# Performance work log

Measured on AMD Instinct MI355X. Metric: run time of the kernel, lower is better.

The kernel has to match this reference:

```python
import jax, jax.numpy as jnp
import numpy as np

GROUPS = 32
EPS = 1e-5


def group_norm(x, w, b):
    # x: [B, C, H, W]
    B, C, H, W = x.shape
    g = x.reshape(B, GROUPS, C // GROUPS, H * W)
    mu = g.mean(axis=(2, 3), keepdims=True)
    var = g.var(axis=(2, 3), keepdims=True)
    g = (g - mu) * jax.lax.rsqrt(var + EPS)
    g = g.reshape(B, C, H, W)
    return g * w[None, :, None, None] + b[None, :, None, None]


def setup_inputs() -> dict:
    key = jax.random.key(0)
    ks = jax.random.split(key, 6)
    B, C, H, W = 4, 512, 64, 64
    s = 1.0 / np.sqrt(C)  # sane init scale for 1x1 conv weights
    return {
        "x": jax.random.normal(ks[0], (B, C, H, W), dtype=jnp.float32),
        "gn_w": jnp.ones((C,), dtype=jnp.float32),
        "gn_b": jnp.zeros((C,), dtype=jnp.float32),
        "wq": jax.random.normal(ks[1], (C, C), dtype=jnp.float32) * s,
        "bq": jnp.zeros((C,), dtype=jnp.float32),
        "wk": jax.random.normal(ks[2], (C, C), dtype=jnp.float32) * s,
        "bk": jnp.zeros((C,), dtype=jnp.float32),
        "wv": jax.random.normal(ks[3], (C, C), dtype=jnp.float32) * s,
        "bv": jnp.zeros((C,), dtype=jnp.float32),
        "wp": jax.random.normal(ks[4], (C, C), dtype=jnp.float32) * s,
        "bp": jnp.zeros((C,), dtype=jnp.float32),
    }


def reference(x, gn_w, gn_b, wq, bq, wk, bk, wv, bv, wp, bp):
    B, C, H, W = x.shape
    h = group_norm(x, gn_w, gn_b)
    # tokens: [B, N, C], N = H*W
    t = h.reshape(B, C, H * W).transpose(0, 2, 1)
    # 1x1 convs == per-token linear: y_d = sum_c w[d,c] * t_c + b_d
    q = jnp.einsum('bnc,dc->bnd', t, wq) + bq
    k = jnp.einsum('bnc,dc->bnd', t, wk) + bk
    v = jnp.einsum('bnc,dc->bnd', t, wv) + bv
    scale = 1.0 / jnp.sqrt(jnp.asarray(C, dtype=x.dtype))
    qk = jnp.einsum('bnd,bmd->bnm', q, k) * scale  # [B, N, N]
    attn = jax.nn.softmax(qk, axis=-1)
    out = jnp.einsum('bnm,bmd->bnd', attn, v)  # [B, N, C]
    proj = jnp.einsum('bnc,dc->bnd', out, wp) + bp
    return x + proj.transpose(0, 2, 1).reshape(B, C, H, W)
```

## Files before the change

kernel.cpp:

```cpp
#include <hip/hip_runtime.h>
#include <stdint.h>

#define B_   4
#define C_   512
#define N_   4096
#define G_   32
#define CPG  16
#define EPS  1e-5f

typedef __attribute__((ext_vector_type(8))) short bf16x8;
typedef __attribute__((ext_vector_type(4))) float f32x4;
typedef __attribute__((ext_vector_type(4))) int   i32x4;

__device__ __forceinline__ unsigned short f2bf(float f){
  union { float f; uint32_t u; } v; v.f = f;
  uint32_t r = v.u + 0x7fffu + ((v.u >> 16) & 1u);
  return (unsigned short)(r >> 16);
}
__device__ __forceinline__ float bf2f(unsigned short h){
  union { uint32_t u; float f; } v; v.u = ((uint32_t)h) << 16;
  return v.f;
}

__device__ __forceinline__ void gload16(const unsigned short* g, unsigned short* l){
  __builtin_amdgcn_global_load_lds(
      (__attribute__((address_space(1))) void*)(g),
      (__attribute__((address_space(3))) void*)(l), 16, 0, 0);
}
__device__ __forceinline__ void gload16i(const signed char* g, signed char* l){
  __builtin_amdgcn_global_load_lds(
      (__attribute__((address_space(1))) void*)(g),
      (__attribute__((address_space(3))) void*)(l), 16, 0, 0);
}

__global__ __launch_bounds__(256) void cvt_kernel(const float* __restrict__ in,
                                                  unsigned short* __restrict__ out, int n){
  int i = (blockIdx.x * 256 + threadIdx.x) * 4;
  if (i < n){
    float4 v = *(const float4*)(in + i);
    out[i+0] = f2bf(v.x); out[i+1] = f2bf(v.y);
    out[i+2] = f2bf(v.z); out[i+3] = f2bf(v.w);
  }
}

__global__ __launch_bounds__(256) void cvt_perm_k(const float* __restrict__ in,
                                                  unsigned short* __restrict__ out, int n){
  int i = (blockIdx.x * 256 + threadIdx.x) * 4;
  if (i < n){
    #pragma unroll
    for (int j = 0; j < 4; j++){
      int idx = i + j;
      int row = idx >> 9, col = idx & 511;
      int o = col & 63;
      int sc = (col & ~63) | (((o & 3) << 4) | (o >> 2));
      out[idx] = f2bf(in[(row << 9) | sc]);
    }
  }
}

__global__ __launch_bounds__(256) void concat_bias_k(const float* __restrict__ bq,
                                                     const float* __restrict__ bk,
                                                     const float* __restrict__ bv,
                                                     float* __restrict__ b){
  int i = blockIdx.x * 256 + threadIdx.x;
  if (i < 1536)
    b[i] = (i < 512) ? bq[i] : ((i < 1024) ? bk[i-512] : bv[i-1024]);
}

__global__ __launch_bounds__(256) void gn_stats_k(const float* __restrict__ x,
                                                  float* __restrict__ stats){
  int bg = blockIdx.x;
  const float* p = x + (size_t)bg * (CPG * N_);
  float s = 0.f, ss = 0.f;
  for (int i = threadIdx.x * 4; i < CPG * N_; i += 256 * 4){
    float4 v = *(const float4*)(p + i);
    s  += v.x + v.y + v.z + v.w;
    ss += v.x*v.x + v.y*v.y + v.z*v.z + v.w*v.w;
  }
  #pragma unroll
  for (int o = 32; o >= 1; o >>= 1){ s += __shfl_xor(s, o); ss += __shfl_xor(ss, o); }
  __shared__ float sb[8];
  int w = threadIdx.x >> 6;
  if ((threadIdx.x & 63) == 0){ sb[w] = s; sb[4+w] = ss; }
  __syncthreads();
  if (threadIdx.x == 0){
    float S  = sb[0]+sb[1]+sb[2]+sb[3];
    float SS = sb[4]+sb[5]+sb[6]+sb[7];
    const float inv = 1.f / (CPG * N_);
    float mu  = S * inv;
    float var = SS * inv - mu * mu;
    stats[bg*2]   = mu;
    stats[bg*2+1] = rsqrtf(var + EPS);
  }
}

__global__ __launch_bounds__(256) void gn_apply_k(const float* __restrict__ x,
                                                  const float* __restrict__ stats,
                                                  const float* __restrict__ gw,
                                                  const float* __restrict__ gb,
                                                  unsigned short* __restrict__ t){
  int b  = blockIdx.z;
  int c0 = blockIdx.y * 64, n0 = blockIdx.x * 64;
  __shared__ float tile[64][65];
  for (int i = threadIdx.x; i < 64*64; i += 256){
    int cl = i >> 6, nl = i & 63;
    int c = c0 + cl;
    int g = c >> 4;
    float mu = stats[(b*G_+g)*2], rs = stats[(b*G_+g)*2+1];
    float v = x[((size_t)b*C_ + c)*N_ + n0 + nl];
    tile[cl][nl] = (v - mu) * rs * gw[c] + gb[c];
  }
  __syncthreads();
  for (int i = threadIdx.x; i < 64*64; i += 256){
    int nl = i >> 6, cl = i & 63;
    t[((size_t)b*N_ + n0 + nl)*C_ + c0 + cl] = f2bf(tile[cl][nl]);
  }
}

__global__ __launch_bounds__(256) void transpose_q8_k(const unsigned short* __restrict__ in,
                                                      signed char* __restrict__ out,
                                                      float invs){
  int r0 = blockIdx.x * 64, c0 = blockIdx.y * 64;
  size_t base_in  = (size_t)blockIdx.z * N_ * 1536;
  size_t base_out = (size_t)blockIdx.z * C_ * N_;
  __shared__ signed char tile[64][68];
  for (int i = threadIdx.x; i < 4096; i += 256){
    int rl = i >> 6, cl = i & 63;
    float v = bf2f(in[base_in + (size_t)(r0+rl)*1536 + c0 + cl]);
    int q = __float2int_rn(v * invs);
    tile[rl][cl] = (signed char)max(-127, min(127, q));
  }
  __syncthreads();
  for (int i = threadIdx.x; i < 4096; i += 256){
    int cl = i >> 6, rl = i & 63;
    int rp = ((rl & 15) << 2) | (rl >> 4);
    out[base_out + (size_t)(c0+cl)*N_ + r0 + rp] = tile[rl][cl];
  }
}

__global__ __launch_bounds__(512, 2) void gemm256_k(const unsigned short* __restrict__ A,
                                                    const unsigned short* __restrict__ Bm,
                                                    unsigned short* __restrict__ Cm,
                                                    int lda, int ldb, int ldc,
                                                    int kper, int zdiv, int Mb,
                                                    long long sA, long long sB,
                                                    long long sC, long long sSp,
                                                    const float* __restrict__ bias,
                                                    float scale, int mode,
                                                    signed char* __restrict__ q8p,
                                                    signed char* __restrict__ k8p,
                                                    float invqs){
  __shared__ unsigned short As[2][256*64];
  __shared__ unsigned short Bs[2][256*64];

  const int tid  = threadIdx.x;
  const int lane = tid & 63, wave = tid >> 6;
  const int wr = wave >> 2, wc = wave & 3;
  const int fr = lane & 15, kl = lane >> 4;
  const int kl8 = kl * 8;
  const int rsw = (fr & 7) << 3;

  const int gx = gridDim.x, gy = gridDim.y;
  const int nwg = gx * gy * gridDim.z;
  int bid = blockIdx.x + gx * (blockIdx.y + gy * blockIdx.z);
  if ((nwg & 7) == 0)
    bid = (bid & 7) * (nwg >> 3) + (bid >> 3);
  const int bx = bid % gx;
  const int tmp2 = bid / gx;
  const int by = tmp2 % gy;
  const int bz = tmp2 / gy;

  const int batch = bz / zdiv;
  const int sp    = bz % zdiv;
  const int koff  = sp * kper;
  const unsigned short* Ab = A  + (size_t)batch*sA + (size_t)bx * 256 * lda + koff;
  const unsigned short* Bb = Bm + (size_t)batch*sB + (size_t)by * 256 * ldb + koff;
  unsigned short*       Cb = Cm + (size_t)batch*sC + (size_t)sp*sSp;

  const int g_row = tid >> 3;
  const int g_col = ((tid & 7) * 8) ^ (((tid >> 3) & 7) << 3);
  const int lw    = wave * 512;

#define STAGE(matG, ld, ldsArr, h, kt) do {                                         \
    const unsigned short* _g0 = (matG) + (size_t)((h)*128 + g_row)*(ld)             \
                                + (size_t)(kt)*64 + g_col;                          \
    gload16(_g0,                    &ldsArr[(kt)&1][(h)*8192 + lw]);                \
    gload16(_g0 + (size_t)64*(ld),  &ldsArr[(kt)&1][(h)*8192 + 4096 + lw]);         \
  } while(0)

  f32x4 acc[8][4];
  #pragma unroll
  for (int m = 0; m < 8; m++)
    #pragma unroll
    for (int n = 0; n < 4; n++)
      acc[m][n] = (f32x4){0.f,0.f,0.f,0.f};

  const int NT = kper >> 6;

  STAGE(Ab, lda, As, 0, 0);  STAGE(Ab, lda, As, 1, 0);
  STAGE(Bb, ldb, Bs, 0, 0);  STAGE(Bb, ldb, Bs, 1, 0);
  STAGE(Bb, ldb, Bs, 0, 1);  STAGE(Bb, ldb, Bs, 1, 1);
  asm volatile("s_waitcnt vmcnt(4)" ::: "memory");
  __builtin_amdgcn_sched_barrier(0);
  __builtin_amdgcn_s_barrier();

  bf16x8 af[4][2], ag[4][2], bfr[2][2], bf2[2][2];

#define RD_A(dst, Tl, mhofs)                                                     \
    _Pragma("unroll")                                                            \
    for (int m = 0; m < 4; m++)                                                  \
      _Pragma("unroll")                                                          \
      for (int kk = 0; kk < 2; kk++)                                             \
        dst[m][kk] = *(const bf16x8*)&Tl[(wr*128 + (mhofs) + m*16 + fr)*64 + ((kk*32 + kl8) ^ rsw)];
#define RD_B(dst, Tl, nofs)                                                      \
    _Pragma("unroll")                                                            \
    for (int n = 0; n < 2; n++)                                                  \
      _Pragma("unroll")                                                          \
      for (int kk = 0; kk < 2; kk++)                                             \
        dst[n][kk] = *(const bf16x8*)&Tl[(wc*64 + (nofs) + n*16 + fr)*64 + ((kk*32 + kl8) ^ rsw)];
#define MFMA16(mbase, nbase, afr, bft)                                           \
    __builtin_amdgcn_s_setprio(1);                                               \
    _Pragma("unroll")                                                            \
    for (int m = 0; m < 4; m++)                                                  \
      _Pragma("unroll")                                                          \
      for (int n = 0; n < 2; n++)                                                \
        _Pragma("unroll")                                                        \
        for (int kk = 0; kk < 2; kk++)                                           \
          acc[(mbase)+m][(nbase)+n] = __builtin_amdgcn_mfma_f32_16x16x32_bf16(   \
              afr[m][kk], bft[n][kk], acc[(mbase)+m][(nbase)+n], 0,0,0);         \
    __builtin_amdgcn_s_setprio(0);
#define BAR_LGKM                                                                 \
    __builtin_amdgcn_s_barrier();                                                \
    asm volatile("s_waitcnt lgkmcnt(0)" ::: "memory");                           \
    __builtin_amdgcn_sched_barrier(0);

  for (int kt = 0; kt < NT; kt += 2){
    const unsigned short* __restrict__ Al0 = As[0];
    const unsigned short* __restrict__ Bl0 = Bs[0];
    const unsigned short* __restrict__ Al1 = As[1];
    const unsigned short* __restrict__ Bl1 = Bs[1];

    RD_A(af, Al0, 0)
    RD_B(bfr, Bl0, 0)
    STAGE(Ab, lda, As, 0, kt+1);
    BAR_LGKM
    MFMA16(0, 0, af, bfr)
    __builtin_amdgcn_s_barrier();

    RD_B(bf2, Bl0, 32)
    STAGE(Ab, lda, As, 1, kt+1);
    BAR_LGKM
    MFMA16(0, 2, af, bf2)
    __builtin_amdgcn_s_barrier();

    RD_A(ag, Al0, 64)
    if (kt+2 < NT) STAGE(Bb, ldb, Bs, 0, kt+2);
    BAR_LGKM
    MFMA16(4, 0, ag, bfr)
    __builtin_amdgcn_s_barrier();

    if (kt+2 < NT){
      STAGE(Bb, ldb, Bs, 1, kt+2);
      asm volatile("s_waitcnt vmcnt(4)" ::: "memory");
    } else {
      asm volatile("s_waitcnt vmcnt(0)" ::: "memory");
    }
    __builtin_amdgcn_sched_barrier(0);
    __builtin_amdgcn_s_barrier();
    __builtin_amdgcn_sched_barrier(0);
    MFMA16(4, 2, ag, bf2)
    __builtin_amdgcn_s_barrier();

    RD_A(af, Al1, 0)
    RD_B(bfr, Bl1, 0)
    if (kt+2 < NT) STAGE(Ab, lda, As, 0, kt+2);
    BAR_LGKM
    MFMA16(0, 0, af, bfr)
    __builtin_amdgcn_s_barrier();

    RD_B(bf2, Bl1, 32)
    if (kt+2 < NT) STAGE(Ab, lda, As, 1, kt+2);
    BAR_LGKM
    MFMA16(0, 2, af, bf2)
    __builtin_amdgcn_s_barrier();

    RD_A(ag, Al1, 64)
    if (kt+3 < NT) STAGE(Bb, ldb, Bs, 0, kt+3);
    BAR_LGKM
    MFMA16(4, 0, ag, bfr)
    __builtin_amdgcn_s_barrier();

    if (kt+3 < NT){
      STAGE(Bb, ldb, Bs, 1, kt+3);
      asm volatile("s_waitcnt vmcnt(4)" ::: "memory");
    } else {
      asm volatile("s_waitcnt vmcnt(0)" ::: "memory");
    }
    __builtin_amdgcn_sched_barrier(0);
    __builtin_amdgcn_s_barrier();
    __builtin_amdgcn_sched_barrier(0);
    MFMA16(4, 2, ag, bf2)
    __builtin_amdgcn_s_barrier();
  }
#undef BAR_LGKM
#undef MFMA16
#undef RD_B
#undef RD_A
#undef STAGE

  const int cr = kl * 4, cc = fr;
  if (mode == 3 && by < 4){
    signed char* dst = (by < 2) ? q8p : k8p;
    const int cb = (by & 1)*256 + wc*64 + cc*4;
    #pragma unroll
    for (int m = 0; m < 8; m++){
      #pragma unroll
      for (int r = 0; r < 4; r++){
        int gr = bx*256 + wr*128 + m*16 + cr + r;
        uint32_t pk = 0;
        #pragma unroll
        for (int n = 0; n < 4; n++){
          int gc = by*256 + wc*64 + n*16 + cc;
          float v = (acc[m][n][r] + bias[gc]) * invqs;
          int q = __float2int_rn(v);
          q = max(-127, min(127, q));
          pk |= (uint32_t)(q & 0xff) << (n*8);
        }
        *(uint32_t*)&dst[(size_t)gr*512 + cb] = pk;
      }
    }
  } else {
    #pragma unroll
    for (int m = 0; m < 8; m++){
      #pragma unroll
      for (int n = 0; n < 4; n++){
        int gc = by*256 + wc*64 + n*16 + cc;
        float bv = (mode == 1 || mode == 3) ? bias[gc] : 0.f;
        #pragma unroll
        for (int r = 0; r < 4; r++){
          int gr = bx*256 + wr*128 + m*16 + cr + r;
          Cb[(size_t)gr*ldc + gc] = f2bf((acc[m][n][r] + bv) * scale);
        }
      }
    }
  }
}

__global__ __launch_bounds__(256, 4) void gemm128i_k(const signed char* __restrict__ A,
                                                     const signed char* __restrict__ Bm,
                                                     void* __restrict__ Cv,
                                                     int lda, int ldb, int ldc,
                                                     int kper, int Mb,
                                                     long long sA, long long sB, long long sC,
                                                     float c1, float c2, int mode,
                                                     float* __restrict__ lpart, int lrows,
                                                     const float* __restrict__ linv){
  __shared__ signed char As[128*128];
  __shared__ signed char Bs[128*128];

  const int tid  = threadIdx.x;
  const int lane = tid & 63, wave = tid >> 6;
  const int wr = wave >> 1, wc = wave & 1;
  const int fr = lane & 15, kl = lane >> 4;
  const int rs = fr & 7;

  const int gx = gridDim.x, gy = gridDim.y;
  const int nwg = gx * gy * gridDim.z;
  int bid = blockIdx.x + gx * (blockIdx.y + gy * blockIdx.z);
  if ((nwg & 7) == 0)
    bid = (bid & 7) * (nwg >> 3) + (bid >> 3);
  const int bx = bid % gx;
  const int tmp2 = bid / gx;
  const int by = tmp2 % gy;
  const int batch = tmp2 / gy;

  const signed char* Ab = A  + (size_t)batch*sA + (size_t)bx * 128 * lda;
  const signed char* Bb = Bm + (size_t)batch*sB + (size_t)by * 128 * ldb;

  const int srow = tid >> 3;
  const int gcol = ((tid & 7) ^ ((tid >> 3) & 7)) * 16;
  const signed char* gA = Ab + (size_t)srow * lda + gcol;
  const signed char* gB = Bb + (size_t)srow * ldb + gcol;
  signed char* lA = &As[srow * 128 + (tid & 7) * 16];
  signed char* lB = &Bs[srow * 128 + (tid & 7) * 16];

  i32x4 acc[4][4];
  #pragma unroll
  for (int m = 0; m < 4; m++)
    #pragma unroll
    for (int n = 0; n < 4; n++)
      acc[m][n] = (i32x4){0,0,0,0};

  const int NT = kper >> 7;

  for (int kt = 0; kt < NT; kt++){
    #pragma unroll
    for (int p = 0; p < 4; p++){
      gload16i(gA + (size_t)(p*32)*lda + (size_t)kt*128, lA + p*4096);
      gload16i(gB + (size_t)(p*32)*ldb + (size_t)kt*128, lB + p*4096);
    }
    __syncthreads();
    i32x4 af[4][2], bf[4][2];
    #pragma unroll
    for (int m = 0; m < 4; m++)
      #pragma unroll
      for (int kk = 0; kk < 2; kk++)
        af[m][kk] = *(const i32x4*)&As[(wr*64 + m*16 + fr)*128 + (((kk*4 + kl) ^ rs) << 4)];
    #pragma unroll
    for (int n = 0; n < 4; n++)
      #pragma unroll
      for (int kk = 0; kk < 2; kk++)
        bf[n][kk] = *(const i32x4*)&Bs[(wc*64 + n*16 + fr)*128 + (((kk*4 + kl) ^ rs) << 4)];
    #pragma unroll
    for (int m = 0; m < 4; m++)
      #pragma unroll
      for (int n = 0; n < 4; n++)
        #pragma unroll
        for (int kk = 0; kk < 2; kk++)
          acc[m][n] = __builtin_amdgcn_mfma_i32_16x16x64_i8(af[m][kk], bf[n][kk], acc[m][n], 0,0,0);
    __syncthreads();
  }

  const int cr = kl * 4, cc = fr;
  if (mode == 2){
    signed char* Cb = (signed char*)Cv + (size_t)batch*sC;
    const int cb = by*128 + wc*64 + cc*4;
    const int slice = by*2 + wc;
    #pragma unroll
    for (int m = 0; m < 4; m++){
      #pragma unroll
      for (int r = 0; r < 4; r++){
        int gr = bx*128 + wr*64 + m*16 + cr + r;
        uint32_t pk = 0;
        int ip = 0;
        #pragma unroll
        for (int n = 0; n < 4; n++){
          float arg = (float)acc[m][n][r] * c1 + c2;
          arg = fminf(arg, 6.99f);
          float p = exp2f(arg);
          int pq = (int)(p + 0.5f);
          pk |= (uint32_t)pq << (n*8);
          ip += pq;
        }
        *(uint32_t*)&Cb[(size_t)gr*ldc + cb] = pk;
        float v = (float)ip;
        v += __shfl_xor(v, 1); v += __shfl_xor(v, 2);
        v += __shfl_xor(v, 4); v += __shfl_xor(v, 8);
        if (cc == 0)
          lpart[(size_t)slice * lrows + batch*Mb + gr] = v;
      }
    }
  } else {
    unsigned short* Cb = (unsigned short*)Cv + (size_t)batch*sC;
    const int cb = by*128 + wc*64 + cc*4;
    #pragma unroll
    for (int m = 0; m < 4; m++){
      #pragma unroll
      for (int r = 0; r < 4; r++){
        int gr = bx*128 + wr*64 + m*16 + cr + r;
        float li = linv[batch*Mb + gr] * c1;
        unsigned short w0 = f2bf((float)acc[m][0][r] * li);
        unsigned short w1 = f2bf((float)acc[m][1][r] * li);
        unsigned short w2 = f2bf((float)acc[m][2][r] * li);
        unsigned short w3 = f2bf((float)acc[m][3][r] * li);
        uint2 pk;
        pk.x = (uint32_t)w0 | ((uint32_t)w1 << 16);
        pk.y = (uint32_t)w2 | ((uint32_t)w3 << 16);
        *(uint2*)&Cb[(size_t)gr*ldc + cb] = pk;
      }
    }
  }
}

__global__ __launch_bounds__(256, 2) void gemm_bt_k(const unsigned short* __restrict__ A,
                                                    const unsigned short* __restrict__ Bm,
                                                    unsigned short* __restrict__ Cm,
                                                    int M, int N, int K, int lda, int ldb,
                                                    const float* __restrict__ bias,
                                                    float scale){
  __shared__ unsigned short As[128*32];
  __shared__ unsigned short Bs[128*32];
  const int tid  = threadIdx.x;
  const int lane = tid & 63, wave = tid >> 6;
  const int wr = wave >> 1, wc = wave & 1;

  const int gx = gridDim.x, gy = gridDim.y;
  const int nwg = gx * gy;
  int bid = blockIdx.x + gx * blockIdx.y;
  if ((nwg & 7) == 0)
    bid = (bid & 7) * (nwg >> 3) + (bid >> 3);
  const int bx = bid % gx;
  const int by = bid / gx;

  const unsigned short* Ab = A  + (size_t)bx * 128 * lda;
  const unsigned short* Bb = Bm + (size_t)by * 128 * ldb;

  f32x4 acc[4][4];
  #pragma unroll
  for (int i = 0; i < 4; i++)
    #pragma unroll
    for (int j = 0; j < 4; j++)
      acc[i][j] = (f32x4){0.f, 0.f, 0.f, 0.f};

  const int ch0  = wave * 2;
  const int srow = ch0 * 16 + (lane >> 2);
  const int scol = (lane & 3) * 8;
  const unsigned short* gA0 = Ab + (size_t)srow * lda + scol;
  const unsigned short* gA1 = gA0 + (size_t)16 * lda;
  const unsigned short* gB0 = Bb + (size_t)srow * ldb + scol;
  const unsigned short* gB1 = gB0 + (size_t)16 * ldb;
  unsigned short* lA0 = &As[ch0 * 512];
  unsigned short* lA1 = &As[ch0 * 512 + 512];
  unsigned short* lB0 = &Bs[ch0 * 512];
  unsigned short* lB1 = &Bs[ch0 * 512 + 512];

  const int fr = lane & 15;
  const int fk = (lane >> 4) * 8;

  for (int k0 = 0; k0 < K; k0 += 32){
    gload16(gA0 + k0, lA0);
    gload16(gA1 + k0, lA1);
    gload16(gB0 + k0, lB0);
    gload16(gB1 + k0, lB1);
    __syncthreads();
    bf16x8 af[4], bfr[4];
    #pragma unroll
    for (int i = 0; i < 4; i++) af[i]  = *(const bf16x8*)&As[(wr*64 + i*16 + fr)*32 + fk];
    #pragma unroll
    for (int j = 0; j < 4; j++) bfr[j] = *(const bf16x8*)&Bs[(wc*64 + j*16 + fr)*32 + fk];
    #pragma unroll
    for (int i = 0; i < 4; i++)
      #pragma unroll
      for (int j = 0; j < 4; j++)
        acc[i][j] = __builtin_amdgcn_mfma_f32_16x16x32_bf16(af[i], bfr[j], acc[i][j], 0, 0, 0);
    __syncthreads();
  }

  const int cr = (lane >> 4) * 4, cc = lane & 15;
  #pragma unroll
  for (int i = 0; i < 4; i++){
    #pragma unroll
    for (int j = 0; j < 4; j++){
      int col = by*128 + wc*64 + j*16 + cc;
      float bv = bias ? bias[col] : 0.f;
      #pragma unroll
      for (int r = 0; r < 4; r++){
        int row = bx*128 + wr*64 + i*16 + cr + r;
        Cm[(size_t)row*N + col] = f2bf((acc[i][j][r] + bv) * scale);
      }
    }
  }
}

__global__ __launch_bounds__(256) void lreduce_k(const float* __restrict__ lpart,
                                                 float* __restrict__ linv,
                                                 int slices, int rows){
  int r = blockIdx.x * 256 + threadIdx.x;
  if (r < rows){
    float s = 0.f;
    for (int i = 0; i < slices; i++) s += lpart[(size_t)i*rows + r];
    linv[r] = 1.f / fmaxf(s, 1.f);
  }
}

__global__ __launch_bounds__(256) void residual_k(const float* __restrict__ x,
                                                  const unsigned short* __restrict__ proj,
                                                  float* __restrict__ out){
  int b  = blockIdx.z;
  int n0 = blockIdx.x * 64, d0 = blockIdx.y * 64;
  __shared__ float tile[64][65];
  for (int i = threadIdx.x; i < 4096; i += 256){
    int nl = i >> 6, dl = i & 63;
    tile[nl][dl] = bf2f(proj[((size_t)b*N_ + n0 + nl)*C_ + d0 + dl]);
  }
  __syncthreads();
  for (int i = threadIdx.x; i < 4096; i += 256){
    int dl = i >> 6, nl = i & 63;
    size_t idx = ((size_t)b*C_ + d0 + dl)*N_ + n0 + nl;
    out[idx] = x[idx] + tile[nl][dl];
  }
}

extern "C" void kernel_launch(void* const* d_in, const int* in_sizes, int n_in,
                              void* d_out, int out_size, void* d_ws, size_t ws_size,
                              hipStream_t stream){
  const float* x   = (const float*)d_in[0];
  const float* gnw = (const float*)d_in[1];
  const float* gnb = (const float*)d_in[2];
  const float* wq  = (const float*)d_in[3];
  const float* bq  = (const float*)d_in[4];
  const float* wk  = (const float*)d_in[5];
  const float* bk  = (const float*)d_in[6];
  const float* wv  = (const float*)d_in[7];
  const float* bv  = (const float*)d_in[8];
  const float* wp  = (const float*)d_in[9];
  const float* bp  = (const float*)d_in[10];
  float* out = (float*)d_out;

  char* ws = (char*)d_ws;
  const int  Mtok = B_ * N_;
  const size_t TSZ   = (size_t)Mtok * C_ * 2;
  const size_t QKVSZ = (size_t)Mtok * 1536 * 2;
  const size_t S8SZ  = (size_t)B_ * N_ * N_;
  const size_t Q8SZ  = (size_t)Mtok * C_;
  size_t off = 0;
  float*          stats = (float*)ws;               off += 4096;
  unsigned short* qkvw = (unsigned short*)(ws+off); off += (size_t)1536 * C_ * 2;
  unsigned short* wpb  = (unsigned short*)(ws+off); off += (size_t)C_ * C_ * 2;
  float*          bqkv = (float*)(ws+off);          off += 1536 * 4 + 2048;
  unsigned short* t    = (unsigned short*)(ws+off); off += TSZ;
  unsigned short* qkv  = (unsigned short*)(ws+off); off += QKVSZ;
  signed char*    S8   = (signed char*)(ws+off);    off += S8SZ;
  float*          lpart = (float*)(ws+off);         off += (size_t)64 * Mtok * 4;
  float*          linv  = (float*)(ws+off);         off += (size_t)Mtok * 4;
  signed char*    q8   = (signed char*)(ws+off);    off += Q8SZ;
  signed char*    k8   = (signed char*)(ws+off);    off += Q8SZ;
  signed char*    vt8  = (signed char*)(ws+off);    off += Q8SZ;

  unsigned short* proj = qkv + 2 * (size_t)Mtok * C_;
  unsigned short* o    = t;

  const float QS    = 6.f / 127.f;
  const float INVQS = 127.f / 6.f;
  const float qkscale = QS * QS * 0.044194173824159216f;
  const float qk_c1 = qkscale * 1.4426950408889634f;
  const float qk_c2 = -0.22478961f;

  const int NW = C_ * C_;
  cvt_kernel<<<NW/1024, 256, 0, stream>>>(wq, qkvw,        NW);
  cvt_kernel<<<NW/1024, 256, 0, stream>>>(wk, qkvw +   NW, NW);
  cvt_kernel<<<NW/1024, 256, 0, stream>>>(wv, qkvw + 2*NW, NW);
  cvt_perm_k<<<NW/1024, 256, 0, stream>>>(wp, wpb,         NW);
  concat_bias_k<<<6, 256, 0, stream>>>(bq, bk, bv, bqkv);

  gn_stats_k<<<B_ * G_, 256, 0, stream>>>(x, stats);
  gn_apply_k<<<dim3(N_/64, C_/64, B_), 256, 0, stream>>>(x, stats, gnw, gnb, t);

  gemm256_k<<<dim3(Mtok/256, 1536/256, 1), 512, 0, stream>>>(
      t, qkvw, qkv, C_, C_, 1536, C_, 1, Mtok, 0,0,0,0, bqkv, 1.f, 3, q8, k8, INVQS);

  transpose_q8_k<<<dim3(N_/64, C_/64, B_), 256, 0, stream>>>(qkv + 1024, vt8, INVQS);

  const long long sQ8 = (long long)N_ * C_;
  const long long sNN = (long long)N_ * N_;
  const long long sNC = (long long)N_ * C_;

  gemm128i_k<<<dim3(N_/128, N_/128, B_), 256, 0, stream>>>(
      q8, k8, S8, C_, C_, N_, C_, N_, sQ8, sQ8, sNN,
      qk_c1, qk_c2, 2, lpart, Mtok, nullptr);

  lreduce_k<<<Mtok/256, 256, 0, stream>>>(lpart, linv, 64, Mtok);

  gemm128i_k<<<dim3(N_/128, C_/128, B_), 256, 0, stream>>>(
      S8, vt8, o, N_, N_, C_, N_, N_, sNN, sQ8, sNC,
      QS, 0.f, 0, nullptr, 0, linv);

  gemm_bt_k<<<dim3(Mtok/128, C_/128, 1), 256, 0, stream>>>(
      o, wpb, proj, Mtok, C_, C_, C_, C_, bp, 1.f);

  residual_k<<<dim3(N_/64, C_/64, B_), 256, 0, stream>>>(x, proj, out);
}
```

Before: 258.7 us.

## Use 256x128 tiles with 512 threads for QK int8 GEMM and fuse prep kernels

Splits the QK^T int8 GEMM into a dedicated kernel with 512-thread blocks covering 256x128 output tiles. Each K tile is then reused across twice as many rows, which halves redundant K loads and the number of workgroups. The weight conversions and bias concat are also merged into one prep kernel, removing four launches. The larger LDS footprint (48KB) and thread count may lower occupancy.

```diff
diff --git a/kernel.cpp b/kernel.cpp
--- a/kernel.cpp
+++ b/kernel.cpp
@@ -33,38 +33,41 @@
       (__attribute__((address_space(3))) void*)(l), 16, 0, 0);
 }
 
-__global__ __launch_bounds__(256) void cvt_kernel(const float* __restrict__ in,
-                                                  unsigned short* __restrict__ out, int n){
-  int i = (blockIdx.x * 256 + threadIdx.x) * 4;
-  if (i < n){
-    float4 v = *(const float4*)(in + i);
-    out[i+0] = f2bf(v.x); out[i+1] = f2bf(v.y);
-    out[i+2] = f2bf(v.z); out[i+3] = f2bf(v.w);
-  }
-}
-
-__global__ __launch_bounds__(256) void cvt_perm_k(const float* __restrict__ in,
-                                                  unsigned short* __restrict__ out, int n){
-  int i = (blockIdx.x * 256 + threadIdx.x) * 4;
-  if (i < n){
-    #pragma unroll
-    for (int j = 0; j < 4; j++){
-      int idx = i + j;
-      int row = idx >> 9, col = idx & 511;
-      int o = col & 63;
-      int sc = (col & ~63) | (((o & 3) << 4) | (o >> 2));
-      out[idx] = f2bf(in[(row << 9) | sc]);
-    }
-  }
-}
-
-__global__ __launch_bounds__(256) void concat_bias_k(const float* __restrict__ bq,
-                                                     const float* __restrict__ bk,
-                                                     const float* __restrict__ bv,
-                                                     float* __restrict__ b){
-  int i = blockIdx.x * 256 + threadIdx.x;
-  if (i < 1536)
-    b[i] = (i < 512) ? bq[i] : ((i < 1024) ? bk[i-512] : bv[i-1024]);
+__global__ __launch_bounds__(256) void prep_k(const float* __restrict__ wq,
+                                              const float* __restrict__ wk,
+                                              const float* __restrict__ wv,
+                                              const float* __restrict__ wp,
+                                              const float* __restrict__ bq,
+                                              const float* __restrict__ bk,
+                                              const float* __restrict__ bv,
+                                              unsigned short* __restrict__ qkvw,
+                                              unsigned short* __restrict__ wpb,
+                                              float* __restrict__ bqkv){
+  const int NW = C_ * C_;
+  int b = blockIdx.x;
+  if (b < 1024){
+    int i = (b * 256 + threadIdx.x) * 4;
+    int region = i / NW;
+    int off = i - region * NW;
+    if (region < 3){
+      const float* src = (region == 0) ? wq : (region == 1) ? wk : wv;
+      float4 v = *(const float4*)(src + off);
+      unsigned short* dst = qkvw + region * NW + off;
+      dst[0] = f2bf(v.x); dst[1] = f2bf(v.y); dst[2] = f2bf(v.z); dst[3] = f2bf(v.w);
+    } else {
+      #pragma unroll
+      for (int j = 0; j < 4; j++){
+        int idx = off + j;
+        int row = idx >> 9, col = idx & 511;
+        int o = col & 63;
+        int sc = (col & ~63) | (((o & 3) << 4) | (o >> 2));
+        wpb[idx] = f2bf(wp[(row << 9) | sc]);
+      }
+    }
+  } else {
+    for (int i = threadIdx.x; i < 1536; i += 256)
+      bqkv[i] = (i < 512) ? bq[i] : ((i < 1024) ? bk[i-512] : bv[i-1024]);
+  }
 }
 
 __global__ __launch_bounds__(256) void gn_stats_k(const float* __restrict__ x,
@@ -346,16 +349,15 @@
   }
 }
 
-__global__ __launch_bounds__(256, 4) void gemm128i_k(const signed char* __restrict__ A,
-                                                     const signed char* __restrict__ Bm,
-                                                     void* __restrict__ Cv,
-                                                     int lda, int ldb, int ldc,
-                                                     int kper, int Mb,
-                                                     long long sA, long long sB, long long sC,
-                                                     float c1, float c2, int mode,
-                                                     float* __restrict__ lpart, int lrows,
-                                                     const float* __restrict__ linv){
-  __shared__ signed char As[128*128];
+__global__ __launch_bounds__(512, 4) void qk256i_k(const signed char* __restrict__ A,
+                                                   const signed char* __restrict__ Bm,
+                                                   signed char* __restrict__ Cv,
+                                                   int lda, int ldb, int ldc,
+                                                   int kper, int Mb,
+                                                   long long sA, long long sB, long long sC,
+                                                   float c1, float c2,
+                                                   float* __restrict__ lpart, int lrows){
+  __shared__ signed char As[256*128];
   __shared__ signed char Bs[128*128];
 
   const int tid  = threadIdx.x;
@@ -374,6 +376,111 @@
   const int by = tmp2 % gy;
   const int batch = tmp2 / gy;
 
+  const signed char* Ab = A  + (size_t)batch*sA + (size_t)bx * 256 * lda;
+  const signed char* Bb = Bm + (size_t)batch*sB + (size_t)by * 128 * ldb;
+
+  const int srow = tid >> 3;
+  const int gcol = ((tid & 7) ^ ((tid >> 3) & 7)) * 16;
+  const signed char* gA = Ab + (size_t)srow * lda + gcol;
+  const signed char* gB = Bb + (size_t)srow * ldb + gcol;
+  signed char* lA = &As[tid * 16];
+  signed char* lB = &Bs[tid * 16];
+
+  i32x4 acc[4][4];
+  #pragma unroll
+  for (int m = 0; m < 4; m++)
+    #pragma unroll
+    for (int n = 0; n < 4; n++)
+      acc[m][n] = (i32x4){0,0,0,0};
+
+  const int NT = kper >> 7;
+
+  for (int kt = 0; kt < NT; kt++){
+    #pragma unroll
+    for (int p = 0; p < 4; p++)
+      gload16i(gA + (size_t)(p*64)*lda + (size_t)kt*128, lA + p*8192);
+    #pragma unroll
+    for (int p = 0; p < 2; p++)
+      gload16i(gB + (size_t)(p*64)*ldb + (size_t)kt*128, lB + p*8192);
+    __syncthreads();
+    i32x4 af[4][2], bf[4][2];
+    #pragma unroll
+    for (int m = 0; m < 4; m++)
+      #pragma unroll
+      for (int kk = 0; kk < 2; kk++)
+        af[m][kk] = *(const i32x4*)&As[(wr*64 + m*16 + fr)*128 + (((kk*4 + kl) ^ rs) << 4)];
+    #pragma unroll
+    for (int n = 0; n < 4; n++)
+      #pragma unroll
+      for (int kk = 0; kk < 2; kk++)
+        bf[n][kk] = *(const i32x4*)&Bs[(wc*64 + n*16 + fr)*128 + (((kk*4 + kl) ^ rs) << 4)];
+    #pragma unroll
+    for (int m = 0; m < 4; m++)
+      #pragma unroll
+      for (int n = 0; n < 4; n++)
+        #pragma unroll
+        for (int kk = 0; kk < 2; kk++)
+          acc[m][n] = __builtin_amdgcn_mfma_i32_16x16x64_i8(af[m][kk], bf[n][kk], acc[m][n], 0,0,0);
+    __syncthreads();
+  }
+
+  const int cr = kl * 4, cc = fr;
+  signed char* Cb = Cv + (size_t)batch*sC;
+  const int cb = by*128 + wc*64 + cc*4;
+  const int slice = by*2 + wc;
+  #pragma unroll
+  for (int m = 0; m < 4; m++){
+    #pragma unroll
+    for (int r = 0; r < 4; r++){
+      int gr = bx*256 + wr*64 + m*16 + cr + r;
+      uint32_t pk = 0;
+      int ip = 0;
+      #pragma unroll
+      for (int n = 0; n < 4; n++){
+        float arg = (float)acc[m][n][r] * c1 + c2;
+        arg = fminf(arg, 6.99f);
+        float p = exp2f(arg);
+        int pq = (int)(p + 0.5f);
+        pk |= (uint32_t)pq << (n*8);
+        ip += pq;
+      }
+      *(uint32_t*)&Cb[(size_t)gr*ldc + cb] = pk;
+      float v = (float)ip;
+      v += __shfl_xor(v, 1); v += __shfl_xor(v, 2);
+      v += __shfl_xor(v, 4); v += __shfl_xor(v, 8);
+      if (cc == 0)
+        lpart[(size_t)slice * lrows + batch*Mb + gr] = v;
+    }
+  }
+}
+
+__global__ __launch_bounds__(256, 4) void gemm128i_k(const signed char* __restrict__ A,
+                                                     const signed char* __restrict__ Bm,
+                                                     void* __restrict__ Cv,
+                                                     int lda, int ldb, int ldc,
+                                                     int kper, int Mb,
+                                                     long long sA, long long sB, long long sC,
+                                                     float c1,
+                                                     const float* __restrict__ linv){
+  __shared__ signed char As[128*128];
+  __shared__ signed char Bs[128*128];
+
+  const int tid  = threadIdx.x;
+  const int lane = tid & 63, wave = tid >> 6;
+  const int wr = wave >> 1, wc = wave & 1;
+  const int fr = lane & 15, kl = lane >> 4;
+  const int rs = fr & 7;
+
+  const int gx = gridDim.x, gy = gridDim.y;
+  const int nwg = gx * gy * gridDim.z;
+  int bid = blockIdx.x + gx * (blockIdx.y + gy * blockIdx.z);
+  if ((nwg & 7) == 0)
+    bid = (bid & 7) * (nwg >> 3) + (bid >> 3);
+  const int bx = bid % gx;
+  const int tmp2 = bid / gx;
+  const int by = tmp2 % gy;
+  const int batch = tmp2 / gy;
+
   const signed char* Ab = A  + (size_t)batch*sA + (size_t)bx * 128 * lda;
   const signed char* Bb = Bm + (size_t)batch*sB + (size_t)by * 128 * ldb;
 
@@ -422,52 +529,22 @@
   }
 
   const int cr = kl * 4, cc = fr;
-  if (mode == 2){
-    signed char* Cb = (signed char*)Cv + (size_t)batch*sC;
-    const int cb = by*128 + wc*64 + cc*4;
-    const int slice = by*2 + wc;
-    #pragma unroll
-    for (int m = 0; m < 4; m++){
-      #pragma unroll
-      for (int r = 0; r < 4; r++){
-        int gr = bx*128 + wr*64 + m*16 + cr + r;
-        uint32_t pk = 0;
-        int ip = 0;
-        #pragma unroll
-        for (int n = 0; n < 4; n++){
-          float arg = (float)acc[m][n][r] * c1 + c2;
-          arg = fminf(arg, 6.99f);
-          float p = exp2f(arg);
-          int pq = (int)(p + 0.5f);
-          pk |= (uint32_t)pq << (n*8);
-          ip += pq;
-        }
-        *(uint32_t*)&Cb[(size_t)gr*ldc + cb] = pk;
-        float v = (float)ip;
-        v += __shfl_xor(v, 1); v += __shfl_xor(v, 2);
-        v += __shfl_xor(v, 4); v += __shfl_xor(v, 8);
-        if (cc == 0)
-          lpart[(size_t)slice * lrows + batch*Mb + gr] = v;
-      }
-    }
-  } else {
-    unsigned short* Cb = (unsigned short*)Cv + (size_t)batch*sC;
-    const int cb = by*128 + wc*64 + cc*4;
-    #pragma unroll
-    for (int m = 0; m < 4; m++){
-      #pragma unroll
-      for (int r = 0; r < 4; r++){
-        int gr = bx*128 + wr*64 + m*16 + cr + r;
-        float li = linv[batch*Mb + gr] * c1;
-        unsigned short w0 = f2bf((float)acc[m][0][r] * li);
-        unsigned short w1 = f2bf((float)acc[m][1][r] * li);
-        unsigned short w2 = f2bf((float)acc[m][2][r] * li);
-        unsigned short w3 = f2bf((float)acc[m][3][r] * li);
-        uint2 pk;
-        pk.x = (uint32_t)w0 | ((uint32_t)w1 << 16);
-        pk.y = (uint32_t)w2 | ((uint32_t)w3 << 16);
-        *(uint2*)&Cb[(size_t)gr*ldc + cb] = pk;
-      }
+  unsigned short* Cb = (unsigned short*)Cv + (size_t)batch*sC;
+  const int cb = by*128 + wc*64 + cc*4;
+  #pragma unroll
+  for (int m = 0; m < 4; m++){
+    #pragma unroll
+    for (int r = 0; r < 4; r++){
+      int gr = bx*128 + wr*64 + m*16 + cr + r;
+      float li = linv[batch*Mb + gr] * c1;
+      unsigned short w0 = f2bf((float)acc[m][0][r] * li);
+      unsigned short w1 = f2bf((float)acc[m][1][r] * li);
+      unsigned short w2 = f2bf((float)acc[m][2][r] * li);
+      unsigned short w3 = f2bf((float)acc[m][3][r] * li);
+      uint2 pk;
+      pk.x = (uint32_t)w0 | ((uint32_t)w1 << 16);
+      pk.y = (uint32_t)w2 | ((uint32_t)w3 << 16);
+      *(uint2*)&Cb[(size_t)gr*ldc + cb] = pk;
     }
   }
 }
@@ -626,12 +703,7 @@
   const float qk_c1 = qkscale * 1.4426950408889634f;
   const float qk_c2 = -0.22478961f;
 
-  const int NW = C_ * C_;
-  cvt_kernel<<<NW/1024, 256, 0, stream>>>(wq, qkvw,        NW);
-  cvt_kernel<<<NW/1024, 256, 0, stream>>>(wk, qkvw +   NW, NW);
-  cvt_kernel<<<NW/1024, 256, 0, stream>>>(wv, qkvw + 2*NW, NW);
-  cvt_perm_k<<<NW/1024, 256, 0, stream>>>(wp, wpb,         NW);
-  concat_bias_k<<<6, 256, 0, stream>>>(bq, bk, bv, bqkv);
+  prep_k<<<1025, 256, 0, stream>>>(wq, wk, wv, wp, bq, bk, bv, qkvw, wpb, bqkv);
 
   gn_stats_k<<<B_ * G_, 256, 0, stream>>>(x, stats);
   gn_apply_k<<<dim3(N_/64, C_/64, B_), 256, 0, stream>>>(x, stats, gnw, gnb, t);
@@ -645,15 +717,15 @@
   const long long sNN = (long long)N_ * N_;
   const long long sNC = (long long)N_ * C_;
 
-  gemm128i_k<<<dim3(N_/128, N_/128, B_), 256, 0, stream>>>(
+  qk256i_k<<<dim3(N_/256, N_/128, B_), 512, 0, stream>>>(
       q8, k8, S8, C_, C_, N_, C_, N_, sQ8, sQ8, sNN,
-      qk_c1, qk_c2, 2, lpart, Mtok, nullptr);
+      qk_c1, qk_c2, lpart, Mtok);
 
   lreduce_k<<<Mtok/256, 256, 0, stream>>>(lpart, linv, 64, Mtok);
 
   gemm128i_k<<<dim3(N_/128, C_/128, B_), 256, 0, stream>>>(
       S8, vt8, o, N_, N_, C_, N_, N_, sNN, sQ8, sNC,
-      QS, 0.f, 0, nullptr, 0, linv);
+      QS, linv);
 
   gemm_bt_k<<<dim3(Mtok/128, C_/128, 1), 256, 0, stream>>>(
       o, wpb, proj, Mtok, C_, C_, C_, C_, bp, 1.f);
```

New measurement: 246.1 us. 1.05x faster.
